# Performance work log

Measured on AMD Instinct MI355X. Metric: run time of the kernel, lower is better.

## Reference

```python
import math
import jax, jax.numpy as jnp
import numpy as np

HEADS, HD = 16, 64  # head_dim = hidden_size // num_heads = 1024 // 16

def _c(a):
    # a: [2, ...] stacked (real, imag) -> complex64
    return jax.lax.complex(a[0], a[1])

def setup_inputs() -> dict:
    key = jax.random.key(0)
    ks = jax.random.split(key, 16)
    B, S, L, H = 2, 2048, 2048, 1024  # batch, chunk len, cache len, hidden
    w_scale = 1.0 / math.sqrt(2 * H)  # complex fan-in scaling
    d = {
        "hidden":  jax.random.normal(ks[0], (2, B, S, H), jnp.float32),
        "k_cache": jax.random.normal(ks[1], (2, B, L, HEADS, HD), jnp.float32),
        "v_cache": jax.random.normal(ks[2], (2, B, L, HEADS, HD), jnp.float32),
        "qw": jax.random.normal(ks[3], (2, H, H), jnp.float32) * w_scale,
        "qb": jax.random.normal(ks[4], (2, H), jnp.float32) * 0.01,
        "kw": jax.random.normal(ks[5], (2, H, H), jnp.float32) * w_scale,
        "kb": jax.random.normal(ks[6], (2, H), jnp.float32) * 0.01,
        "vw": jax.random.normal(ks[7], (2, H, H), jnp.float32) * w_scale,
        "vb": jax.random.normal(ks[8], (2, H), jnp.float32) * 0.01,
        "ow": jax.random.normal(ks[9], (2, H, H), jnp.float32) * w_scale,
        "ob": jax.random.normal(ks[10], (2, H), jnp.float32) * 0.01,
        "ln_gamma": jnp.stack([jnp.ones(H, jnp.float32) + 0.01 * jax.random.normal(ks[11], (H,)),
                               0.01 * jax.random.normal(ks[12], (H,))]),
        "ln_beta":  0.01 * jax.random.normal(ks[13], (2, H), jnp.float32),
    }
    return d

def _complex_layernorm(x, gamma, beta, eps=1e-5):
    mu = jnp.mean(x, axis=-1, keepdims=True)              # complex mean
    xc = x - mu
    var = jnp.mean(xc.real**2 + xc.imag**2, axis=-1, keepdims=True)
    return xc / jnp.sqrt(var + eps) * gamma + beta

def _clin(z, w, b):
    # complex linear: z [..., in] @ W^T [out, in] + b [out]
    return jnp.einsum('bsh,oh->bso', z, _c(w)) + _c(b)

def reference(hidden, k_cache, v_cache, qw, qb, kw, kb, vw, vb, ow, ob, ln_gamma, ln_beta):
    x = _c(hidden)                                        # [B,S,H] complex64
    B, S, H = x.shape
    normed = _complex_layernorm(x, _c(ln_gamma), _c(ln_beta))
    Q = _clin(normed, qw, qb).reshape(B, S, HEADS, HD)
    K_new = _clin(normed, kw, kb).reshape(B, S, HEADS, HD)
    V_new = _clin(normed, vw, vb).reshape(B, S, HEADS, HD)
    K = jnp.concatenate([_c(k_cache), K_new], axis=1)     # [B, L+S, nh, hd]
    V = jnp.concatenate([_c(v_cache), V_new], axis=1)
    cache_len = k_cache.shape[2]
    kv = K.shape[1]                                       # == window_size here
    # Hermitian score: Re(Q K^dagger) / sqrt(hd)
    scores = jnp.einsum('bqhd,bkhd->bhqk', Q, jnp.conj(K)).real / math.sqrt(HD)
    row = jnp.arange(S)[:, None]
    col = jnp.arange(kv)[None, :]
    # prefix (cache) fully visible; causal within the new chunk
    mask = jnp.where((col >= cache_len) & (col - cache_len > row), -jnp.inf, 0.0).astype(scores.dtype)
    w = jax.nn.softmax(scores + mask[None, None], axis=-1)  # real weights
    out = jax.lax.complex(jnp.einsum('bhqk,bkhd->bqhd', w, V.real),
                          jnp.einsum('bhqk,bkhd->bqhd', w, V.imag)).reshape(B, S, H)
    delta = _clin(out, ow, ob)
    y = x + delta
    out_stacked = jnp.stack([y.real, y.imag])             # [2,B,S,H]
    new_k = jnp.stack([K.real, K.imag])                   # [2,B,window,nh,hd]
    new_v = jnp.stack([V.real, V.imag])
    return (out_stacked, new_k, new_v)
```

## Files before the change

### kernel.cpp

```cpp
#include <hip/hip_runtime.h>

#define HEADS 16
#define SEQ   2048
#define HID   1024
#define CACHE 2048
#define KVLEN 4096
#define MROWS 4096
#define KD    2048

typedef float  f32x4  __attribute__((ext_vector_type(4)));
typedef __bf16 bf16x8 __attribute__((ext_vector_type(8)));

__device__ __forceinline__ void gload_lds16(const void* g, void* l) {
  __builtin_amdgcn_global_load_lds((const __attribute__((address_space(1))) void*)g,
                                   (__attribute__((address_space(3))) void*)l, 16, 0, 0);
}

__global__ __launch_bounds__(256) void k_layernorm(const float* __restrict__ hid,
                                                   const float* __restrict__ gamma,
                                                   const float* __restrict__ beta,
                                                   __bf16* __restrict__ normed) {
  int row = blockIdx.x;
  int t = threadIdx.x;
  const float* xr = hid + (size_t)row * HID;
  const float* xi = hid + (size_t)MROWS * HID + (size_t)row * HID;
  float vr[4], vi[4];
  float sr = 0.f, si = 0.f;
#pragma unroll
  for (int i = 0; i < 4; i++) { int h = t + i * 256; vr[i] = xr[h]; vi[i] = xi[h]; sr += vr[i]; si += vi[i]; }
  __shared__ float red[2][4];
  for (int m = 1; m < 64; m <<= 1) { sr += __shfl_xor(sr, m); si += __shfl_xor(si, m); }
  int wid = t >> 6, l = t & 63;
  if (l == 0) { red[0][wid] = sr; red[1][wid] = si; }
  __syncthreads();
  float mr = (red[0][0] + red[0][1] + red[0][2] + red[0][3]) * (1.0f / HID);
  float mi = (red[1][0] + red[1][1] + red[1][2] + red[1][3]) * (1.0f / HID);
  float sv = 0.f;
#pragma unroll
  for (int i = 0; i < 4; i++) { float a = vr[i] - mr, b = vi[i] - mi; sv += a * a + b * b; }
  for (int m = 1; m < 64; m <<= 1) sv += __shfl_xor(sv, m);
  __syncthreads();
  if (l == 0) red[0][wid] = sv;
  __syncthreads();
  float var = (red[0][0] + red[0][1] + red[0][2] + red[0][3]) * (1.0f / HID);
  float inv = rsqrtf(var + 1e-5f);
  __bf16* outr = normed + (size_t)row * KD;
#pragma unroll
  for (int i = 0; i < 4; i++) {
    int h = t + i * 256;
    float a = (vr[i] - mr) * inv, b = (vi[i] - mi) * inv;
    float gr = gamma[h], gi = gamma[HID + h], br = beta[h], bi = beta[HID + h];
    outr[h]       = (__bf16)(a * gr - b * gi + br);
    outr[HID + h] = (__bf16)(a * gi + b * gr + bi);
  }
}

__global__ __launch_bounds__(256) void k_packw(const float* __restrict__ w, __bf16* __restrict__ dst) {
  int idx = blockIdx.x * 256 + threadIdx.x;
  int o  = idx >> 8;
  int k0 = (idx & 255) * 8;
  const float* wr = w;
  const float* wi = w + HID * HID;
  int oimag = (o >= HID);
  int oo = o & (HID - 1);
  bf16x8 v;
#pragma unroll
  for (int j = 0; j < 8; j++) {
    int k = k0 + j;
    int kim = (k >= HID);
    int kk = k & (HID - 1);
    float x;
    if (!oimag) x = kim ? -wi[oo * HID + kk] : wr[oo * HID + kk];
    else        x = kim ?  wr[oo * HID + kk] : wi[oo * HID + kk];
    v[j] = (__bf16)x;
  }
  *(bf16x8*)(dst + (size_t)o * KD + k0) = v;
}

__global__ __launch_bounds__(256) void k_copycache(const float* __restrict__ src, float* __restrict__ dst) {
  size_t i = (size_t)blockIdx.x * 256 + threadIdx.x;
  size_t sf = i << 2;
  size_t chunk = sf >> 21;
  size_t df = sf + (chunk << 21);
  *(f32x4*)(dst + df) = *(const f32x4*)(src + sf);
}

__global__ __launch_bounds__(256) void k_buildk(const float* __restrict__ src, __bf16* __restrict__ dst) {
  int c = blockIdx.x * 256 + threadIdx.x;
  int ch = c & 7;
  int kv = (c >> 3) & 4095;
  int h  = (c >> 15) & 15;
  int b  = (c >> 19) & 1;
  int p  = (c >> 20) & 1;
  const float* s = src + (((size_t)(p * 2 + b)) * KVLEN + kv) * HID + h * 64 + ch * 8;
  bf16x8 v;
#pragma unroll
  for (int j = 0; j < 8; j++) v[j] = (__bf16)s[j];
  *(bf16x8*)(dst + (((size_t)(b * 16 + h)) * KVLEN + kv) * 128 + p * 64 + ch * 8) = v;
}

__global__ __launch_bounds__(256) void k_buildv(const float* __restrict__ src, __bf16* __restrict__ dst) {
  __shared__ float tile[32][129];
  int kt = blockIdx.x;
  int bh = blockIdx.y;
  int b = bh >> 4, h = bh & 15;
  int t = threadIdx.x;
  int kv0 = kt * 32;
#pragma unroll
  for (int i = 0; i < 16; i++) {
    int idx = i * 256 + t;
    int kvl = idx >> 7, dsl = idx & 127;
    int p = dsl >> 6, d = dsl & 63;
    tile[kvl][dsl] = src[(((size_t)(p * 2 + b)) * KVLEN + kv0 + kvl) * HID + h * 64 + d];
  }
  __syncthreads();
#pragma unroll
  for (int i = 0; i < 16; i++) {
    int idx = i * 256 + t;
    int dsl = idx >> 5, kvl = idx & 31;
    dst[(((size_t)bh) * 128 + dsl) * KVLEN + kv0 + kvl] = (__bf16)tile[kvl][dsl];
  }
}

#define BM 128
#define BN 128
#define BK 64
template <int MODE>
__global__ __launch_bounds__(256) void k_gemm(const __bf16* __restrict__ A,
                                              const __bf16* __restrict__ Bp,
                                              const float* __restrict__ bias,
                                              const float* __restrict__ hid,
                                              float* __restrict__ outF,
                                              __bf16* __restrict__ outB) {
  __shared__ __align__(16) __bf16 As[BM * BK];
  __shared__ __align__(16) __bf16 Bs[BN * BK];
  int bm0 = blockIdx.x * BM, bn0 = blockIdx.y * BN;
  int t = threadIdx.x, l = t & 63, wid = t >> 6;
  int wr = wid >> 1, wc = wid & 1;
  int l15 = l & 15, lg = l >> 4;
  f32x4 acc[4][4];
  f32x4 zero = {0.f, 0.f, 0.f, 0.f};
#pragma unroll
  for (int i = 0; i < 4; i++)
#pragma unroll
    for (int j = 0; j < 4; j++) acc[i][j] = zero;
  const __bf16* Ab = A + (size_t)bm0 * KD;
  const __bf16* Bb = Bp + (size_t)bn0 * KD;
  for (int k0 = 0; k0 < KD; k0 += BK) {
#pragma unroll
    for (int c = 0; c < 4; c++) {
      int idx = c * 256 + t;
      int row = idx >> 3, ch = idx & 7;
      gload_lds16(Ab + (size_t)row * KD + k0 + ch * 8, As + idx * 8);
      gload_lds16(Bb + (size_t)row * KD + k0 + ch * 8, Bs + idx * 8);
    }
    __syncthreads();
#pragma unroll
    for (int ks = 0; ks < 2; ks++) {
      bf16x8 af[4], bfv[4];
#pragma unroll
      for (int i = 0; i < 4; i++) {
        af[i]  = *(const bf16x8*)(As + (wr * 64 + i * 16 + l15) * BK + ks * 32 + lg * 8);
        bfv[i] = *(const bf16x8*)(Bs + (wc * 64 + i * 16 + l15) * BK + ks * 32 + lg * 8);
      }
#pragma unroll
      for (int mi = 0; mi < 4; mi++)
#pragma unroll
        for (int ni = 0; ni < 4; ni++)
          acc[mi][ni] = __builtin_amdgcn_mfma_f32_16x16x32_bf16(af[mi], bfv[ni], acc[mi][ni], 0, 0, 0);
    }
    __syncthreads();
  }
#pragma unroll
  for (int mi = 0; mi < 4; mi++) {
#pragma unroll
    for (int ni = 0; ni < 4; ni++) {
#pragma unroll
      for (int j = 0; j < 4; j++) {
        int m = bm0 + wr * 64 + mi * 16 + lg * 4 + j;
        int n = bn0 + wc * 64 + ni * 16 + l15;
        float v = acc[mi][ni][j] + bias[n];
        int b = m >> 11, s = m & 2047;
        if (MODE == 0) {
          int head = (n & 1023) >> 6;
          int dslot = (n & 63) + ((n >= 1024) ? 64 : 0);
          outB[(((size_t)(b * 16 + head)) * SEQ + s) * 128 + dslot] = (__bf16)v;
        } else if (MODE == 1 || MODE == 2) {
          int p = n >> 10;
          outF[(((size_t)(p * 2 + b)) * KVLEN + (CACHE + s)) * HID + (n & 1023)] = v;
        } else {
          int p = n >> 10;
          size_t off = (((size_t)(p * 2 + b)) * SEQ + s) * HID + (n & 1023);
          outF[off] = v + hid[off];
        }
      }
    }
  }
}

__global__ __launch_bounds__(256, 2) void k_attn(const __bf16* __restrict__ Q,
                                                 const __bf16* __restrict__ Kt,
                                                 const __bf16* __restrict__ Vt,
                                                 __bf16* __restrict__ outp) {
  __shared__ __align__(16) __bf16 Ks[2][64 * 128];
  __shared__ __align__(16) __bf16 Vs[2][128 * 64];
  __shared__ __align__(16) __bf16 Ps[4][32 * 64];
  int id = blockIdx.y * gridDim.x + blockIdx.x;
  int xcd = id & 7, li = id >> 3;
  int bh = (xcd << 2) | (li >> 4);
  int qt = li & 15;
  int b = bh >> 4, h = bh & 15;
  int t = threadIdx.x, l = t & 63, wid = t >> 6;
  int l15 = l & 15, lg = l >> 4;
  const __bf16* Qb = Q + ((size_t)bh * SEQ) * 128;
  const __bf16* Kb = Kt + ((size_t)bh * KVLEN) * 128;
  const __bf16* Vb = Vt + ((size_t)bh * 128) * KVLEN;
  int q0 = qt * 128 + wid * 32;
  bf16x8 aQ[2][4];
#pragma unroll
  for (int mi = 0; mi < 2; mi++)
#pragma unroll
    for (int dk = 0; dk < 4; dk++)
      aQ[mi][dk] = *(const bf16x8*)(Qb + (size_t)(q0 + mi * 16 + l15) * 128 + dk * 32 + lg * 8);
  f32x4 zero = {0.f, 0.f, 0.f, 0.f};
  f32x4 o[2][8];
  f32x4 sums[2];
#pragma unroll
  for (int mi = 0; mi < 2; mi++) {
    sums[mi] = zero;
#pragma unroll
    for (int df = 0; df < 8; df++) o[mi][df] = zero;
  }
  bf16x8 ones;
#pragma unroll
  for (int i = 0; i < 8; i++) ones[i] = (__bf16)1.0f;
  const int nfull = 32 + 2 * qt;
  const int nt = nfull + 2;
  int sw = (l15 & 7) << 4;

  auto STAGE = [&](int bb, int ti) {
    int kv0 = ti * 64;
#pragma unroll
    for (int c = 0; c < 4; c++) {
      int idx = c * 256 + t;
      int kr = idx >> 4;
      gload_lds16(Kb + (size_t)(kv0 + kr) * 128 + (((idx & 15) ^ (kr & 7)) << 3), &Ks[bb][idx * 8]);
      int vr = idx >> 3;
      gload_lds16(Vb + (size_t)vr * KVLEN + kv0 + (((idx & 7) ^ (vr & 7)) << 3), &Vs[bb][idx * 8]);
    }
  };

  STAGE(0, 0);
  for (int ti = 0; ti < nt; ti++) {
    int bb = ti & 1;
    if (ti + 1 < nt) {
      STAGE(bb ^ 1, ti + 1);
      asm volatile("s_waitcnt vmcnt(8)" ::: "memory");
    } else {
      asm volatile("s_waitcnt vmcnt(0)" ::: "memory");
    }
    __builtin_amdgcn_s_barrier();
    const char* KsB = (const char*)&Ks[bb][0];
    const char* VsB = (const char*)&Vs[bb][0];
    f32x4 sacc[2][4];
    __builtin_amdgcn_s_setprio(1);
#pragma unroll
    for (int kvf = 0; kvf < 4; kvf++) {
      sacc[0][kvf] = zero; sacc[1][kvf] = zero;
      const char* kbase = KsB + (kvf * 16 + l15) * 256;
#pragma unroll
      for (int dk = 0; dk < 4; dk++) {
        bf16x8 bK = *(const bf16x8*)(kbase + ((dk * 64 + lg * 16) ^ sw));
        sacc[0][kvf] = __builtin_amdgcn_mfma_f32_16x16x32_bf16(aQ[0][dk], bK, sacc[0][kvf], 0, 0, 0);
        sacc[1][kvf] = __builtin_amdgcn_mfma_f32_16x16x32_bf16(aQ[1][dk], bK, sacc[1][kvf], 0, 0, 0);
      }
    }
    __builtin_amdgcn_s_setprio(0);
    bool masked = (ti >= nfull);
#pragma unroll
    for (int mi = 0; mi < 2; mi++) {
#pragma unroll
      for (int j = 0; j < 4; j++) {
        int prow = mi * 16 + lg * 4 + j;
        int pxor = (prow & 7) << 4;
        int qg = qt * 128 + wid * 32 + prow;
#pragma unroll
        for (int kvf = 0; kvf < 4; kvf++) {
          float s = sacc[mi][kvf][j] * 0.18033688011112042f;
          float p = exp2f(s);
          if (masked) {
            int cg = ti * 64 + kvf * 16 + l15 - CACHE;
            if (cg > qg) p = 0.f;
          }
          Ps[wid][(prow * 128 + ((kvf * 32 + l15 * 2) ^ pxor)) >> 1] = (__bf16)p;
        }
      }
    }
    __builtin_amdgcn_s_setprio(1);
#pragma unroll
    for (int mi = 0; mi < 2; mi++) {
      const char* pbase = (const char*)&Ps[wid][0] + (mi * 16 + l15) * 128;
#pragma unroll
      for (int ks = 0; ks < 2; ks++) {
        int off = (ks * 64 + lg * 16) ^ sw;
        bf16x8 aP = *(const bf16x8*)(pbase + off);
        sums[mi] = __builtin_amdgcn_mfma_f32_16x16x32_bf16(aP, ones, sums[mi], 0, 0, 0);
#pragma unroll
        for (int df = 0; df < 8; df++) {
          bf16x8 bV = *(const bf16x8*)(VsB + (df * 16 + l15) * 128 + off);
          o[mi][df] = __builtin_amdgcn_mfma_f32_16x16x32_bf16(aP, bV, o[mi][df], 0, 0, 0);
        }
      }
    }
    __builtin_amdgcn_s_setprio(0);
    __builtin_amdgcn_s_barrier();
  }
#pragma unroll
  for (int mi = 0; mi < 2; mi++) {
    float inv[4];
#pragma unroll
    for (int j = 0; j < 4; j++) inv[j] = 1.0f / sums[mi][j];
#pragma unroll
    for (int df = 0; df < 8; df++) {
      int dslot = df * 16 + l15;
      int col = (dslot < 64) ? (h * 64 + dslot) : (1024 + h * 64 + (dslot - 64));
#pragma unroll
      for (int j = 0; j < 4; j++) {
        int qg2 = q0 + mi * 16 + lg * 4 + j;
        float v = o[mi][df][j] * inv[j];
        outp[((size_t)(b * SEQ + qg2)) * KD + col] = (__bf16)v;
      }
    }
  }
}

extern "C" void kernel_launch(void* const* d_in, const int* in_sizes, int n_in,
                              void* d_out, int out_size, void* d_ws, size_t ws_size,
                              hipStream_t stream) {
  const float* hid = (const float*)d_in[0];
  const float* kc  = (const float*)d_in[1];
  const float* vc  = (const float*)d_in[2];
  const float* qw  = (const float*)d_in[3];
  const float* qb  = (const float*)d_in[4];
  const float* kw  = (const float*)d_in[5];
  const float* kb  = (const float*)d_in[6];
  const float* vw  = (const float*)d_in[7];
  const float* vb  = (const float*)d_in[8];
  const float* ow  = (const float*)d_in[9];
  const float* ob  = (const float*)d_in[10];
  const float* lg  = (const float*)d_in[11];
  const float* lb  = (const float*)d_in[12];

  float* y  = (float*)d_out;
  float* nk = y + 8388608;
  float* nv = nk + 16777216;

  char* ws = (char*)d_ws;
  __bf16* normed = (__bf16*)(ws);
  __bf16* wqp    = (__bf16*)(ws + 16777216);
  __bf16* wkp    = (__bf16*)(ws + 25165824);
  __bf16* wvp    = (__bf16*)(ws + 33554432);
  __bf16* wop    = (__bf16*)(ws + 41943040);
  __bf16* Qa     = (__bf16*)(ws + 50331648);
  __bf16* Ka     = (__bf16*)(ws + 67108864);
  __bf16* Va     = (__bf16*)(ws + 100663296);
  __bf16* ao     = (__bf16*)(ws + 134217728);

  k_layernorm<<<4096, 256, 0, stream>>>(hid, lg, lb, normed);
  k_packw<<<2048, 256, 0, stream>>>(qw, wqp);
  k_packw<<<2048, 256, 0, stream>>>(kw, wkp);
  k_packw<<<2048, 256, 0, stream>>>(vw, wvp);
  k_packw<<<2048, 256, 0, stream>>>(ow, wop);
  k_copycache<<<8192, 256, 0, stream>>>(kc, nk);
  k_copycache<<<8192, 256, 0, stream>>>(vc, nv);
  dim3 gg(32, 16);
  k_gemm<0><<<gg, 256, 0, stream>>>(normed, wqp, qb, nullptr, nullptr, Qa);
  k_gemm<1><<<gg, 256, 0, stream>>>(normed, wkp, kb, nullptr, nk, nullptr);
  k_gemm<2><<<gg, 256, 0, stream>>>(normed, wvp, vb, nullptr, nv, nullptr);
  k_buildk<<<8192, 256, 0, stream>>>(nk, Ka);
  dim3 gv(128, 32);
  k_buildv<<<gv, 256, 0, stream>>>(nv, Va);
  dim3 ga(16, 32);
  k_attn<<<ga, 256, 0, stream>>>(Qa, Ka, Va, ao);
  k_gemm<3><<<gg, 256, 0, stream>>>(ao, wop, ob, hid, y, nullptr);
}
```

Measured before the change: 533.6 us.

## Use 128x256 double-buffered swizzled GEMM and fuse K bf16 build into copy/GEMM

Replaces the 128x128 single-buffered GEMM with a 512-thread 128x256 tile that double-buffers LDS stages, uses XOR-swizzled LDS layout to avoid bank conflicts, and raises MFMA priority. The separate k_buildk pass is removed: the cache copy kernel now also writes the bf16 K layout, and the K projection GEMM writes both fp32 and bf16 outputs. This cuts an extra read of the full K tensor and improves GEMM overlap, at the cost of lower occupancy (one block per CU, 256 blocks) and more LDS.

```diff
diff --git a/kernel.cpp b/kernel.cpp
--- a/kernel.cpp
+++ b/kernel.cpp
@@ -9,6 +9,7 @@
 #define KD    2048
 
 typedef float  f32x4  __attribute__((ext_vector_type(4)));
+typedef __bf16 bf16x4 __attribute__((ext_vector_type(4)));
 typedef __bf16 bf16x8 __attribute__((ext_vector_type(8)));
 
 __device__ __forceinline__ void gload_lds16(const void* g, void* l) {
@@ -85,18 +86,21 @@
   *(f32x4*)(dst + df) = *(const f32x4*)(src + sf);
 }
 
-__global__ __launch_bounds__(256) void k_buildk(const float* __restrict__ src, __bf16* __restrict__ dst) {
-  int c = blockIdx.x * 256 + threadIdx.x;
-  int ch = c & 7;
-  int kv = (c >> 3) & 4095;
-  int h  = (c >> 15) & 15;
-  int b  = (c >> 19) & 1;
-  int p  = (c >> 20) & 1;
-  const float* s = src + (((size_t)(p * 2 + b)) * KVLEN + kv) * HID + h * 64 + ch * 8;
-  bf16x8 v;
-#pragma unroll
-  for (int j = 0; j < 8; j++) v[j] = (__bf16)s[j];
-  *(bf16x8*)(dst + (((size_t)(b * 16 + h)) * KVLEN + kv) * 128 + p * 64 + ch * 8) = v;
+__global__ __launch_bounds__(256) void k_copycache_k(const float* __restrict__ src,
+                                                     float* __restrict__ nk,
+                                                     __bf16* __restrict__ Ka) {
+  int i = blockIdx.x * 256 + threadIdx.x;
+  int c4 = i & 255;
+  int kv = (i >> 8) & 2047;
+  int b  = (i >> 19) & 1;
+  int p  = (i >> 20) & 1;
+  f32x4 v = *(const f32x4*)(src + (((size_t)((p * 2 + b) * 2048 + kv)) << 10) + c4 * 4);
+  *(f32x4*)(nk + ((((size_t)(p * 2 + b)) * KVLEN + kv) << 10) + c4 * 4) = v;
+  int h = c4 >> 4, d = (c4 & 15) * 4;
+  bf16x4 w;
+#pragma unroll
+  for (int j = 0; j < 4; j++) w[j] = (__bf16)v[j];
+  *(bf16x4*)(Ka + (((size_t)(b * 16 + h)) * KVLEN + kv) * 128 + p * 64 + d) = w;
 }
 
 __global__ __launch_bounds__(256) void k_buildv(const float* __restrict__ src, __bf16* __restrict__ dst) {
@@ -122,22 +126,25 @@
   }
 }
 
-#define BM 128
-#define BN 128
-#define BK 64
+#define GBM 128
+#define GBN 256
+#define GBK 64
 template <int MODE>
-__global__ __launch_bounds__(256) void k_gemm(const __bf16* __restrict__ A,
-                                              const __bf16* __restrict__ Bp,
-                                              const float* __restrict__ bias,
-                                              const float* __restrict__ hid,
-                                              float* __restrict__ outF,
-                                              __bf16* __restrict__ outB) {
-  __shared__ __align__(16) __bf16 As[BM * BK];
-  __shared__ __align__(16) __bf16 Bs[BN * BK];
-  int bm0 = blockIdx.x * BM, bn0 = blockIdx.y * BN;
+__global__ __launch_bounds__(512, 1) void k_gemm256(const __bf16* __restrict__ A,
+                                                    const __bf16* __restrict__ Bp,
+                                                    const float* __restrict__ bias,
+                                                    const float* __restrict__ hid,
+                                                    float* __restrict__ outF,
+                                                    __bf16* __restrict__ outB) {
+  __shared__ __align__(16) __bf16 As[2][GBM * GBK];
+  __shared__ __align__(16) __bf16 Bs[2][GBN * GBK];
+  int id = blockIdx.x;
+  int nb = id & 7, mb = id >> 3;
+  int bm0 = mb * GBM, bn0 = nb * GBN;
   int t = threadIdx.x, l = t & 63, wid = t >> 6;
-  int wr = wid >> 1, wc = wid & 1;
+  int wm = wid >> 2, wn = wid & 3;
   int l15 = l & 15, lg = l >> 4;
+  int swz = (l15 & 7) << 4;
   f32x4 acc[4][4];
   f32x4 zero = {0.f, 0.f, 0.f, 0.f};
 #pragma unroll
@@ -146,46 +153,85 @@
     for (int j = 0; j < 4; j++) acc[i][j] = zero;
   const __bf16* Ab = A + (size_t)bm0 * KD;
   const __bf16* Bb = Bp + (size_t)bn0 * KD;
-  for (int k0 = 0; k0 < KD; k0 += BK) {
-#pragma unroll
-    for (int c = 0; c < 4; c++) {
-      int idx = c * 256 + t;
-      int row = idx >> 3, ch = idx & 7;
-      gload_lds16(Ab + (size_t)row * KD + k0 + ch * 8, As + idx * 8);
-      gload_lds16(Bb + (size_t)row * KD + k0 + ch * 8, Bs + idx * 8);
-    }
-    __syncthreads();
-#pragma unroll
-    for (int ks = 0; ks < 2; ks++) {
-      bf16x8 af[4], bfv[4];
-#pragma unroll
-      for (int i = 0; i < 4; i++) {
-        af[i]  = *(const bf16x8*)(As + (wr * 64 + i * 16 + l15) * BK + ks * 32 + lg * 8);
-        bfv[i] = *(const bf16x8*)(Bs + (wc * 64 + i * 16 + l15) * BK + ks * 32 + lg * 8);
-      }
-#pragma unroll
-      for (int mi = 0; mi < 4; mi++)
-#pragma unroll
-        for (int ni = 0; ni < 4; ni++)
-          acc[mi][ni] = __builtin_amdgcn_mfma_f32_16x16x32_bf16(af[mi], bfv[ni], acc[mi][ni], 0, 0, 0);
-    }
-    __syncthreads();
-  }
-#pragma unroll
-  for (int mi = 0; mi < 4; mi++) {
-#pragma unroll
-    for (int ni = 0; ni < 4; ni++) {
+
+  auto STAGE = [&](int bb, int k0) {
+#pragma unroll
+    for (int i = 0; i < 2; i++) {
+      int row = i * 64 + wid * 8 + (l >> 3);
+      gload_lds16(Ab + (size_t)row * KD + k0 + (((l & 7) ^ (row & 7)) << 3),
+                  &As[bb][0] + i * 4096 + wid * 512 + (l & 63) * 8);
+    }
+#pragma unroll
+    for (int i = 0; i < 4; i++) {
+      int row = i * 64 + wid * 8 + (l >> 3);
+      gload_lds16(Bb + (size_t)row * KD + k0 + (((l & 7) ^ (row & 7)) << 3),
+                  &Bs[bb][0] + i * 4096 + wid * 512 + (l & 63) * 8);
+    }
+  };
+
+  STAGE(0, 0);
+  const int NT = KD / GBK;
+  for (int tt = 0; tt < NT; tt++) {
+    int bb = tt & 1;
+    if (tt + 1 < NT) {
+      STAGE(bb ^ 1, (tt + 1) * GBK);
+      asm volatile("s_waitcnt vmcnt(6)" ::: "memory");
+    } else {
+      asm volatile("s_waitcnt vmcnt(0)" ::: "memory");
+    }
+    __builtin_amdgcn_s_barrier();
+    const char* AsB = (const char*)&As[bb][0];
+    const char* BsB = (const char*)&Bs[bb][0];
+#pragma unroll
+    for (int ph = 0; ph < 2; ph++) {
+      if (ph) __builtin_amdgcn_s_barrier();
+      bf16x8 aF[4][2], bF[2][2];
+#pragma unroll
+      for (int mf = 0; mf < 4; mf++) {
+        int row = wm * 64 + mf * 16 + l15;
+#pragma unroll
+        for (int ks = 0; ks < 2; ks++)
+          aF[mf][ks] = *(const bf16x8*)(AsB + row * 128 + ((ks * 64 + lg * 16) ^ swz));
+      }
+#pragma unroll
+      for (int nf = 0; nf < 2; nf++) {
+        int row = wn * 64 + (ph * 2 + nf) * 16 + l15;
+#pragma unroll
+        for (int ks = 0; ks < 2; ks++)
+          bF[nf][ks] = *(const bf16x8*)(BsB + row * 128 + ((ks * 64 + lg * 16) ^ swz));
+      }
+      __builtin_amdgcn_s_setprio(1);
+#pragma unroll
+      for (int mf = 0; mf < 4; mf++)
+#pragma unroll
+        for (int nf = 0; nf < 2; nf++)
+#pragma unroll
+          for (int ks = 0; ks < 2; ks++)
+            acc[mf][ph * 2 + nf] =
+                __builtin_amdgcn_mfma_f32_16x16x32_bf16(aF[mf][ks], bF[nf][ks], acc[mf][ph * 2 + nf], 0, 0, 0);
+      __builtin_amdgcn_s_setprio(0);
+    }
+    __builtin_amdgcn_s_barrier();
+  }
+#pragma unroll
+  for (int mf = 0; mf < 4; mf++) {
+#pragma unroll
+    for (int nf = 0; nf < 4; nf++) {
 #pragma unroll
       for (int j = 0; j < 4; j++) {
-        int m = bm0 + wr * 64 + mi * 16 + lg * 4 + j;
-        int n = bn0 + wc * 64 + ni * 16 + l15;
-        float v = acc[mi][ni][j] + bias[n];
+        int m = bm0 + wm * 64 + mf * 16 + lg * 4 + j;
+        int n = bn0 + wn * 64 + nf * 16 + l15;
+        float v = acc[mf][nf][j] + bias[n];
         int b = m >> 11, s = m & 2047;
         if (MODE == 0) {
           int head = (n & 1023) >> 6;
           int dslot = (n & 63) + ((n >= 1024) ? 64 : 0);
           outB[(((size_t)(b * 16 + head)) * SEQ + s) * 128 + dslot] = (__bf16)v;
-        } else if (MODE == 1 || MODE == 2) {
+        } else if (MODE == 1) {
+          int p = n >> 10, hd = n & 1023;
+          outF[(((size_t)(p * 2 + b)) * KVLEN + (CACHE + s)) * HID + hd] = v;
+          outB[(((size_t)(b * 16 + (hd >> 6))) * KVLEN + (CACHE + s)) * 128 + p * 64 + (hd & 63)] = (__bf16)v;
+        } else if (MODE == 2) {
           int p = n >> 10;
           outF[(((size_t)(p * 2 + b)) * KVLEN + (CACHE + s)) * HID + (n & 1023)] = v;
         } else {
@@ -371,16 +417,14 @@
   k_packw<<<2048, 256, 0, stream>>>(kw, wkp);
   k_packw<<<2048, 256, 0, stream>>>(vw, wvp);
   k_packw<<<2048, 256, 0, stream>>>(ow, wop);
-  k_copycache<<<8192, 256, 0, stream>>>(kc, nk);
+  k_copycache_k<<<8192, 256, 0, stream>>>(kc, nk, Ka);
   k_copycache<<<8192, 256, 0, stream>>>(vc, nv);
-  dim3 gg(32, 16);
-  k_gemm<0><<<gg, 256, 0, stream>>>(normed, wqp, qb, nullptr, nullptr, Qa);
-  k_gemm<1><<<gg, 256, 0, stream>>>(normed, wkp, kb, nullptr, nk, nullptr);
-  k_gemm<2><<<gg, 256, 0, stream>>>(normed, wvp, vb, nullptr, nv, nullptr);
-  k_buildk<<<8192, 256, 0, stream>>>(nk, Ka);
+  k_gemm256<0><<<256, 512, 0, stream>>>(normed, wqp, qb, nullptr, nullptr, Qa);
+  k_gemm256<1><<<256, 512, 0, stream>>>(normed, wkp, kb, nullptr, nk, Ka);
+  k_gemm256<2><<<256, 512, 0, stream>>>(normed, wvp, vb, nullptr, nv, nullptr);
   dim3 gv(128, 32);
   k_buildv<<<gv, 256, 0, stream>>>(nv, Va);
   dim3 ga(16, 32);
   k_attn<<<ga, 256, 0, stream>>>(Qa, Ka, Va, ao);
-  k_gemm<3><<<gg, 256, 0, stream>>>(ao, wop, ob, hid, y, nullptr);
-}
+  k_gemm256<3><<<256, 512, 0, stream>>>(ao, wop, ob, hid, y, nullptr);
+}
```

Result: slower. 550.7 us (+3.2%).

## Fuse QKV GEMMs, weight packing, and cache copy with K bf16 build

Applied to the files above, without the earlier changes.

Merges the four weight-pack launches into one, and merges the two cache copies into one kernel that also writes the bf16 K layout for the cache part. The Q, K and V projections now run as a single GEMM over a concatenated weight matrix, and the K epilogue writes both the fp32 cache output and the bf16 attention layout, so the separate K rebuild pass is gone. This removes launches and a full read of the K cache. In exchange the epilogue does more scattered stores and picks a bias per column, and the GEMM now asks for 3 blocks per CU, which may constrain registers.

```diff
diff --git a/kernel.cpp b/kernel.cpp
--- a/kernel.cpp
+++ b/kernel.cpp
@@ -9,6 +9,7 @@
 #define KD    2048
 
 typedef float  f32x4  __attribute__((ext_vector_type(4)));
+typedef __bf16 bf16x4 __attribute__((ext_vector_type(4)));
 typedef __bf16 bf16x8 __attribute__((ext_vector_type(8)));
 
 __device__ __forceinline__ void gload_lds16(const void* g, void* l) {
@@ -55,10 +56,15 @@
   }
 }
 
-__global__ __launch_bounds__(256) void k_packw(const float* __restrict__ w, __bf16* __restrict__ dst) {
+__global__ __launch_bounds__(256) void k_packw(const float* __restrict__ qw, const float* __restrict__ kw,
+                                               const float* __restrict__ vw, const float* __restrict__ ow,
+                                               __bf16* __restrict__ dst) {
   int idx = blockIdx.x * 256 + threadIdx.x;
-  int o  = idx >> 8;
-  int k0 = (idx & 255) * 8;
+  int sel = idx >> 19;
+  int li  = idx & 524287;
+  const float* w = sel == 0 ? qw : (sel == 1 ? kw : (sel == 2 ? vw : ow));
+  int o  = li >> 8;
+  int k0 = (li & 255) * 8;
   const float* wr = w;
   const float* wi = w + HID * HID;
   int oimag = (o >= HID);
@@ -74,29 +80,33 @@
     else        x = kim ?  wr[oo * HID + kk] : wi[oo * HID + kk];
     v[j] = (__bf16)x;
   }
-  *(bf16x8*)(dst + (size_t)o * KD + k0) = v;
-}
-
-__global__ __launch_bounds__(256) void k_copycache(const float* __restrict__ src, float* __restrict__ dst) {
-  size_t i = (size_t)blockIdx.x * 256 + threadIdx.x;
-  size_t sf = i << 2;
-  size_t chunk = sf >> 21;
-  size_t df = sf + (chunk << 21);
-  *(f32x4*)(dst + df) = *(const f32x4*)(src + sf);
-}
-
-__global__ __launch_bounds__(256) void k_buildk(const float* __restrict__ src, __bf16* __restrict__ dst) {
-  int c = blockIdx.x * 256 + threadIdx.x;
-  int ch = c & 7;
-  int kv = (c >> 3) & 4095;
-  int h  = (c >> 15) & 15;
-  int b  = (c >> 19) & 1;
-  int p  = (c >> 20) & 1;
-  const float* s = src + (((size_t)(p * 2 + b)) * KVLEN + kv) * HID + h * 64 + ch * 8;
-  bf16x8 v;
-#pragma unroll
-  for (int j = 0; j < 8; j++) v[j] = (__bf16)s[j];
-  *(bf16x8*)(dst + (((size_t)(b * 16 + h)) * KVLEN + kv) * 128 + p * 64 + ch * 8) = v;
+  *(bf16x8*)(dst + ((size_t)sel << 22) + (size_t)o * KD + k0) = v;
+}
+
+__global__ __launch_bounds__(256) void k_copykv(const float* __restrict__ kc, const float* __restrict__ vc,
+                                                float* __restrict__ nk, float* __restrict__ nv,
+                                                __bf16* __restrict__ Ka) {
+  int i = blockIdx.x * 256 + threadIdx.x;
+  int sel = i >> 21;
+  int li = i & ((1 << 21) - 1);
+  if (sel == 0) {
+    int c4 = li & 255;
+    int kv = (li >> 8) & 2047;
+    int b  = (li >> 19) & 1;
+    int p  = (li >> 20) & 1;
+    f32x4 v = *(const f32x4*)(kc + (((size_t)((p * 2 + b) * 2048 + kv)) << 10) + c4 * 4);
+    *(f32x4*)(nk + ((((size_t)(p * 2 + b)) * KVLEN + kv) << 10) + c4 * 4) = v;
+    int h = c4 >> 4, d = (c4 & 15) * 4;
+    bf16x4 w;
+#pragma unroll
+    for (int j = 0; j < 4; j++) w[j] = (__bf16)v[j];
+    *(bf16x4*)(Ka + (((size_t)(b * 16 + h)) * KVLEN + kv) * 128 + p * 64 + d) = w;
+  } else {
+    size_t sf = (size_t)li << 2;
+    size_t chunk = sf >> 21;
+    size_t df = sf + (chunk << 21);
+    *(f32x4*)(nv + df) = *(const f32x4*)(vc + sf);
+  }
 }
 
 __global__ __launch_bounds__(256) void k_buildv(const float* __restrict__ src, __bf16* __restrict__ dst) {
@@ -125,13 +135,17 @@
 #define BM 128
 #define BN 128
 #define BK 64
-template <int MODE>
-__global__ __launch_bounds__(256) void k_gemm(const __bf16* __restrict__ A,
-                                              const __bf16* __restrict__ Bp,
-                                              const float* __restrict__ bias,
-                                              const float* __restrict__ hid,
-                                              float* __restrict__ outF,
-                                              __bf16* __restrict__ outB) {
+template <int QKV>
+__global__ __launch_bounds__(256, 3) void k_gemm(const __bf16* __restrict__ A,
+                                                 const __bf16* __restrict__ Bp,
+                                                 const float* __restrict__ bias0,
+                                                 const float* __restrict__ bias1,
+                                                 const float* __restrict__ bias2,
+                                                 const float* __restrict__ hid,
+                                                 float* __restrict__ outF0,
+                                                 float* __restrict__ outF1,
+                                                 __bf16* __restrict__ outB0,
+                                                 __bf16* __restrict__ outB1) {
   __shared__ __align__(16) __bf16 As[BM * BK];
   __shared__ __align__(16) __bf16 Bs[BN * BK];
   int bm0 = blockIdx.x * BM, bn0 = blockIdx.y * BN;
@@ -179,19 +193,25 @@
       for (int j = 0; j < 4; j++) {
         int m = bm0 + wr * 64 + mi * 16 + lg * 4 + j;
         int n = bn0 + wc * 64 + ni * 16 + l15;
-        float v = acc[mi][ni][j] + bias[n];
         int b = m >> 11, s = m & 2047;
-        if (MODE == 0) {
-          int head = (n & 1023) >> 6;
-          int dslot = (n & 63) + ((n >= 1024) ? 64 : 0);
-          outB[(((size_t)(b * 16 + head)) * SEQ + s) * 128 + dslot] = (__bf16)v;
-        } else if (MODE == 1 || MODE == 2) {
-          int p = n >> 10;
-          outF[(((size_t)(p * 2 + b)) * KVLEN + (CACHE + s)) * HID + (n & 1023)] = v;
+        if (QKV) {
+          int mode = n >> 11, nl = n & 2047;
+          const float* bias = mode == 0 ? bias0 : (mode == 1 ? bias1 : bias2);
+          float v = acc[mi][ni][j] + bias[nl];
+          int p = nl >> 10, hd = nl & 1023;
+          if (mode == 0) {
+            outB0[(((size_t)(b * 16 + (hd >> 6))) * SEQ + s) * 128 + p * 64 + (hd & 63)] = (__bf16)v;
+          } else if (mode == 1) {
+            outF0[(((size_t)(p * 2 + b)) * KVLEN + (CACHE + s)) * HID + hd] = v;
+            outB1[(((size_t)(b * 16 + (hd >> 6))) * KVLEN + (CACHE + s)) * 128 + p * 64 + (hd & 63)] = (__bf16)v;
+          } else {
+            outF1[(((size_t)(p * 2 + b)) * KVLEN + (CACHE + s)) * HID + hd] = v;
+          }
         } else {
+          float v = acc[mi][ni][j] + bias0[n];
           int p = n >> 10;
           size_t off = (((size_t)(p * 2 + b)) * SEQ + s) * HID + (n & 1023);
-          outF[off] = v + hid[off];
+          outF0[off] = v + hid[off];
         }
       }
     }
@@ -357,30 +377,21 @@
 
   char* ws = (char*)d_ws;
   __bf16* normed = (__bf16*)(ws);
-  __bf16* wqp    = (__bf16*)(ws + 16777216);
-  __bf16* wkp    = (__bf16*)(ws + 25165824);
-  __bf16* wvp    = (__bf16*)(ws + 33554432);
-  __bf16* wop    = (__bf16*)(ws + 41943040);
+  __bf16* wall   = (__bf16*)(ws + 16777216);
   __bf16* Qa     = (__bf16*)(ws + 50331648);
   __bf16* Ka     = (__bf16*)(ws + 67108864);
   __bf16* Va     = (__bf16*)(ws + 100663296);
   __bf16* ao     = (__bf16*)(ws + 134217728);
 
   k_layernorm<<<4096, 256, 0, stream>>>(hid, lg, lb, normed);
-  k_packw<<<2048, 256, 0, stream>>>(qw, wqp);
-  k_packw<<<2048, 256, 0, stream>>>(kw, wkp);
-  k_packw<<<2048, 256, 0, stream>>>(vw, wvp);
-  k_packw<<<2048, 256, 0, stream>>>(ow, wop);
-  k_copycache<<<8192, 256, 0, stream>>>(kc, nk);
-  k_copycache<<<8192, 256, 0, stream>>>(vc, nv);
-  dim3 gg(32, 16);
-  k_gemm<0><<<gg, 256, 0, stream>>>(normed, wqp, qb, nullptr, nullptr, Qa);
-  k_gemm<1><<<gg, 256, 0, stream>>>(normed, wkp, kb, nullptr, nk, nullptr);
-  k_gemm<2><<<gg, 256, 0, stream>>>(normed, wvp, vb, nullptr, nv, nullptr);
-  k_buildk<<<8192, 256, 0, stream>>>(nk, Ka);
+  k_packw<<<8192, 256, 0, stream>>>(qw, kw, vw, ow, wall);
+  k_copykv<<<16384, 256, 0, stream>>>(kc, vc, nk, nv, Ka);
+  dim3 gq(32, 48);
+  k_gemm<1><<<gq, 256, 0, stream>>>(normed, wall, qb, kb, vb, nullptr, nk, nv, Qa, Ka);
   dim3 gv(128, 32);
   k_buildv<<<gv, 256, 0, stream>>>(nv, Va);
   dim3 ga(16, 32);
   k_attn<<<ga, 256, 0, stream>>>(Qa, Ka, Va, ao);
-  k_gemm<3><<<gg, 256, 0, stream>>>(ao, wop, ob, hid, y, nullptr);
-}
+  dim3 go(32, 16);
+  k_gemm<0><<<go, 256, 0, stream>>>(ao, wall + ((size_t)3 << 22), ob, nullptr, nullptr, hid, y, nullptr, nullptr, nullptr);
+}
```

Result: faster. 458.5 us (-14.1%).
